# Performance work log

Measured on AMD Instinct MI355X. Metric: run time of the kernel, lower is better.

## Reference

```python
import jax, jax.numpy as jnp
import numpy as np

N_NODES = 100000


def gcn_layer(x, edge_index, W, b):
    """PyG GCNConv: h = D^-1/2 (A+I) D^-1/2 (x W) + b, scatter-sum aggregation."""
    n = x.shape[0]
    h = x @ W  # [N, out]
    loop = jnp.arange(n, dtype=edge_index.dtype)
    src = jnp.concatenate([edge_index[0], loop])  # [E+N]
    dst = jnp.concatenate([edge_index[1], loop])
    deg = jax.ops.segment_sum(jnp.ones_like(dst, dtype=h.dtype), dst, num_segments=n)
    dinv = jnp.where(deg > 0, jax.lax.rsqrt(deg), 0.0)
    norm = dinv[src] * dinv[dst]  # [E+N]
    msg = h[src] * norm[:, None]  # gather + scale (largest intermediate)
    out = jax.ops.segment_sum(msg, dst, num_segments=n)
    return out + b


def setup_inputs() -> dict:
    key = jax.random.key(0)
    k = jax.random.split(key, 8)
    in_dim, hid_dim, out_dim = 128, 64, 112
    E = 1600000
    x = jax.random.normal(k[0], (N_NODES, in_dim), dtype=jnp.float32)
    edge_index = jax.random.randint(k[1], (2, E), 0, N_NODES, dtype=jnp.int32)
    s1 = 1.0 / np.sqrt(in_dim)
    s2 = 1.0 / np.sqrt(hid_dim)
    return {
        "x": x,
        "edge_index": edge_index,
        "W1": jax.random.uniform(k[2], (in_dim, hid_dim), jnp.float32, -s1, s1),
        "b1": jnp.zeros((hid_dim,), jnp.float32),
        "W2": jax.random.uniform(k[3], (hid_dim, hid_dim), jnp.float32, -s2, s2),
        "b2": jnp.zeros((hid_dim,), jnp.float32),
        "W3": jax.random.uniform(k[4], (hid_dim, out_dim), jnp.float32, -s2, s2),
        "b3": jnp.zeros((out_dim,), jnp.float32),
    }


def reference(x, edge_index, W1, b1, W2, b2, W3, b3):
    # eval mode: dropout is identity
    h = jax.nn.relu(gcn_layer(x, edge_index, W1, b1))
    h = jax.nn.relu(gcn_layer(h, edge_index, W2, b2))
    return gcn_layer(h, edge_index, W3, b3)
```

## Files before the change

kernel.cpp:

```cpp
#include <hip/hip_runtime.h>
#include <hip/hip_fp16.h>
#include <math.h>


#define IN_DIM 128
#define HID 64
#define OUT_DIM 112
#define SCAN_TILE 1024
#define LSHIFT 7
#define LMASK 127
#define MAXBUCK 1024
#define CHUNK 8192

__global__ __launch_bounds__(256) void coarse_hist_kernel(const int* __restrict__ dst,
                                                          int* __restrict__ H,
                                                          int E, int nbuck) {
  __shared__ int hist[MAXBUCK];
  for (int i = threadIdx.x; i < nbuck; i += 256) hist[i] = 0;
  __syncthreads();
  int lo = blockIdx.x * CHUNK;
  int hi = min(E, lo + CHUNK);
  for (int i = lo + threadIdx.x; i < hi; i += 256)
    atomicAdd(&hist[dst[i] >> LSHIFT], 1);
  __syncthreads();
  int* Hrow = &H[(size_t)blockIdx.x * nbuck];
  for (int i = threadIdx.x; i < nbuck; i += 256) Hrow[i] = hist[i];
}

__global__ __launch_bounds__(256) void btotal_kernel(const int* __restrict__ H,
                                                     int* __restrict__ btotal,
                                                     int nchunk, int nbuck) {
  int wv = threadIdx.x >> 6, lane = threadIdx.x & 63;
  int b = blockIdx.x * 4 + wv;
  if (b >= nbuck) return;
  int s = 0;
  for (int c = lane; c < nchunk; c += 64) s += H[(size_t)c * nbuck + b];
#pragma unroll
  for (int off = 1; off < 64; off <<= 1) s += __shfl_xor(s, off);
  if (lane == 0) btotal[b] = s;
}

__global__ __launch_bounds__(1024) void bbase_scan_kernel(const int* __restrict__ btotal,
                                                          int* __restrict__ bbase, int nbuck) {
  __shared__ int sh[1024];
  int t = threadIdx.x;
  int v = (t < nbuck) ? btotal[t] : 0;
  sh[t] = v;
  __syncthreads();
  for (int off = 1; off < 1024; off <<= 1) {
    int u = (t >= off) ? sh[t - off] : 0;
    __syncthreads();
    sh[t] += u;
    __syncthreads();
  }
  if (t < nbuck) bbase[t] = sh[t] - v;
  if (t == 1023) bbase[nbuck] = sh[1023];
}

__global__ __launch_bounds__(256) void chunk_offset_kernel(int* __restrict__ H,
                                                           const int* __restrict__ bbase,
                                                           int nchunk, int nbuck) {
  int wv = threadIdx.x >> 6, lane = threadIdx.x & 63;
  int b = blockIdx.x * 4 + wv;
  if (b >= nbuck) return;
  int run = bbase[b];
  for (int c0 = 0; c0 < nchunk; c0 += 64) {
    int c = c0 + lane;
    int v = (c < nchunk) ? H[(size_t)c * nbuck + b] : 0;
    int incl = v;
#pragma unroll
    for (int off = 1; off < 64; off <<= 1) {
      int u = __shfl_up(incl, off);
      if (lane >= off) incl += u;
    }
    if (c < nchunk) H[(size_t)c * nbuck + b] = run + incl - v;
    run += __shfl(incl, 63);
  }
}

__global__ __launch_bounds__(256) void coarse_scatter_kernel(const int* __restrict__ src,
                                                             const int* __restrict__ dst,
                                                             const int* __restrict__ H,
                                                             int* __restrict__ packed,
                                                             int E, int nbuck) {
  __shared__ int cur[MAXBUCK];
  const int* Hrow = &H[(size_t)blockIdx.x * nbuck];
  for (int i = threadIdx.x; i < nbuck; i += 256) cur[i] = Hrow[i];
  __syncthreads();
  int lo = blockIdx.x * CHUNK;
  int hi = min(E, lo + CHUNK);
  for (int i = lo + threadIdx.x; i < hi; i += 256) {
    int s = src[i], d = dst[i];
    int b = d >> LSHIFT;
    int pos = atomicAdd(&cur[b], 1);
    packed[pos] = (s << LSHIFT) | (d & LMASK);
  }
}

__global__ __launch_bounds__(256) void fine_count_kernel(const int* __restrict__ packed,
                                                         const int* __restrict__ bbase,
                                                         int* __restrict__ cnt, int n) {
  int b = blockIdx.x;
  __shared__ int hist[128];
  int t = threadIdx.x;
  if (t < 128) hist[t] = 0;
  __syncthreads();
  int e0 = bbase[b], e1 = bbase[b + 1];
  for (int e = e0 + t; e < e1; e += 256) atomicAdd(&hist[packed[e] & LMASK], 1);
  __syncthreads();
  int node = b * 128 + t;
  if (t < 128 && node < n) cnt[node] = hist[t];
}

__global__ __launch_bounds__(256) void fine_scatter_kernel(const int* __restrict__ packed,
                                                           const int* __restrict__ bbase,
                                                           const int* __restrict__ row_start,
                                                           int* __restrict__ ssrc, int n) {
  int b = blockIdx.x;
  __shared__ int cur[128];
  int t = threadIdx.x;
  if (t < 128) {
    int node = b * 128 + t;
    cur[t] = (node < n) ? row_start[node] : 0;
  }
  __syncthreads();
  int e0 = bbase[b], e1 = bbase[b + 1];
  for (int e = e0 + t; e < e1; e += 256) {
    int p = packed[e];
    int slot = atomicAdd(&cur[p & LMASK], 1);
    ssrc[slot] = p >> LSHIFT;
  }
}

__global__ __launch_bounds__(256) void dinv_kernel(const int* __restrict__ cnt,
                                                   float* __restrict__ dinv, int n) {
  int i = blockIdx.x * 256 + threadIdx.x;
  if (i < n) dinv[i] = 1.0f / sqrtf((float)(cnt[i] + 1));
}


__global__ __launch_bounds__(256) void scan_partial_kernel(const int* __restrict__ cnt,
                                                           int* __restrict__ blocksum,
                                                           int n) {
  int t = threadIdx.x;
  int base = blockIdx.x * SCAN_TILE + t * 4;
  int s = 0;
  if (base + 4 <= n) {
    int4 v = *reinterpret_cast<const int4*>(&cnt[base]);
    s = v.x + v.y + v.z + v.w;
  } else {
    for (int i = 0; i < 4; ++i)
      if (base + i < n) s += cnt[base + i];
  }
#pragma unroll
  for (int off = 1; off < 64; off <<= 1) s += __shfl_xor(s, off);
  __shared__ int wsum[4];
  int lane = t & 63, wv = t >> 6;
  if (lane == 0) wsum[wv] = s;
  __syncthreads();
  if (t == 0) blocksum[blockIdx.x] = wsum[0] + wsum[1] + wsum[2] + wsum[3];
}

__global__ __launch_bounds__(1024) void scan_blocksums_kernel(int* __restrict__ blocksum,
                                                              int* __restrict__ total_out,
                                                              int nb) {
  __shared__ int sh[1024];
  int t = threadIdx.x;
  int v = (t < nb) ? blocksum[t] : 0;
  sh[t] = v;
  __syncthreads();
  for (int off = 1; off < 1024; off <<= 1) {
    int u = (t >= off) ? sh[t - off] : 0;
    __syncthreads();
    sh[t] += u;
    __syncthreads();
  }
  if (t < nb) blocksum[t] = sh[t] - v;
  if (t == 1023) *total_out = sh[1023];
}

__global__ __launch_bounds__(256) void scan_final_kernel(const int* __restrict__ cnt,
                                                         const int* __restrict__ blocksum,
                                                         int* __restrict__ row_start, int n) {
  int t = threadIdx.x;
  int base = blockIdx.x * SCAN_TILE + t * 4;
  int v0 = 0, v1 = 0, v2 = 0, v3 = 0;
  if (base + 4 <= n) {
    int4 v = *reinterpret_cast<const int4*>(&cnt[base]);
    v0 = v.x; v1 = v.y; v2 = v.z; v3 = v.w;
  } else {
    if (base + 0 < n) v0 = cnt[base + 0];
    if (base + 1 < n) v1 = cnt[base + 1];
    if (base + 2 < n) v2 = cnt[base + 2];
    if (base + 3 < n) v3 = cnt[base + 3];
  }
  int s = v0 + v1 + v2 + v3;
  __shared__ int sh[256];
  sh[t] = s;
  __syncthreads();
  for (int off = 1; off < 256; off <<= 1) {
    int u = (t >= off) ? sh[t - off] : 0;
    __syncthreads();
    sh[t] += u;
    __syncthreads();
  }
  int run = blocksum[blockIdx.x] + sh[t] - s;
  int p0 = run, p1 = run + v0, p2 = p1 + v1, p3 = p2 + v2;
  if (base + 4 <= n) {
    *reinterpret_cast<int4*>(&row_start[base]) = make_int4(p0, p1, p2, p3);
  } else {
    if (base + 0 < n) row_start[base + 0] = p0;
    if (base + 1 < n) row_start[base + 1] = p1;
    if (base + 2 < n) row_start[base + 2] = p2;
    if (base + 3 < n) row_start[base + 3] = p3;
  }
}

template <int K, int C, int BK, bool DINV, bool BIAS, bool OUTH>
__global__ __launch_bounds__(256, 4) void gemm_scale_kernel(const float* __restrict__ X,
                                                            const float* __restrict__ W,
                                                            const float* __restrict__ dinv,
                                                            const float* __restrict__ bias,
                                                            void* __restrict__ G, int n) {
  constexpr int Cp = ((C + 63) / 64) * 64;
  constexpr int CQ = Cp / 4;
  constexpr int RG = 256 / CQ;
  constexpr int RPB = RG * 4;
  constexpr int XP = BK + 4;
  constexpr int XQ = BK / 4;
  constexpr int NXQ = RPB * XQ;
  constexpr int NWQ = BK * CQ;

  __shared__ float Xs[RPB * XP];
  __shared__ float Ws[BK * Cp];

  const int tid = threadIdx.x;
  const int rbase = blockIdx.x * RPB;
  const int ct = tid % CQ, rt = tid / CQ;
  const int c0 = ct * 4, r0 = rt * 4;

  float acc[4][4];
#pragma unroll
  for (int a = 0; a < 4; ++a)
#pragma unroll
    for (int b = 0; b < 4; ++b) acc[a][b] = 0.f;

  for (int kb = 0; kb < K; kb += BK) {
    if (kb > 0) __syncthreads();
#pragma unroll
    for (int q = tid; q < NXQ; q += 256) {
      int r = q / XQ, j = q % XQ;
      int grow = rbase + r;
      if (grow >= n) grow = n - 1;
      *reinterpret_cast<float4*>(&Xs[r * XP + j * 4]) =
          *reinterpret_cast<const float4*>(&X[(size_t)grow * K + kb + j * 4]);
    }
#pragma unroll
    for (int q = tid; q < NWQ; q += 256) {
      int k = q / CQ, cq = q % CQ, c = cq * 4;
      float4 v = make_float4(0.f, 0.f, 0.f, 0.f);
      if (c < C) v = *reinterpret_cast<const float4*>(&W[(size_t)(kb + k) * C + c]);
      *reinterpret_cast<float4*>(&Ws[k * Cp + c]) = v;
    }
    __syncthreads();

#pragma unroll 2
    for (int k = 0; k < BK; k += 4) {
      float4 w0 = *reinterpret_cast<const float4*>(&Ws[(k + 0) * Cp + c0]);
      float4 w1 = *reinterpret_cast<const float4*>(&Ws[(k + 1) * Cp + c0]);
      float4 w2 = *reinterpret_cast<const float4*>(&Ws[(k + 2) * Cp + c0]);
      float4 w3 = *reinterpret_cast<const float4*>(&Ws[(k + 3) * Cp + c0]);
#pragma unroll
      for (int rr = 0; rr < 4; ++rr) {
        float4 xv = *reinterpret_cast<const float4*>(&Xs[(r0 + rr) * XP + k]);
        acc[rr][0] = fmaf(xv.w, w3.x, fmaf(xv.z, w2.x, fmaf(xv.y, w1.x, fmaf(xv.x, w0.x, acc[rr][0]))));
        acc[rr][1] = fmaf(xv.w, w3.y, fmaf(xv.z, w2.y, fmaf(xv.y, w1.y, fmaf(xv.x, w0.y, acc[rr][1]))));
        acc[rr][2] = fmaf(xv.w, w3.z, fmaf(xv.z, w2.z, fmaf(xv.y, w1.z, fmaf(xv.x, w0.z, acc[rr][2]))));
        acc[rr][3] = fmaf(xv.w, w3.w, fmaf(xv.z, w2.w, fmaf(xv.y, w1.w, fmaf(xv.x, w0.w, acc[rr][3]))));
      }
    }
  }

#pragma unroll
  for (int rr = 0; rr < 4; ++rr) {
    int row = rbase + r0 + rr;
    if (row < n && c0 < C) {
      float s = DINV ? dinv[row] : 1.0f;
      float4 v;
      v.x = acc[rr][0] * s;
      v.y = acc[rr][1] * s;
      v.z = acc[rr][2] * s;
      v.w = acc[rr][3] * s;
      if (BIAS) {
        float4 bv = *reinterpret_cast<const float4*>(&bias[c0]);
        v.x += bv.x; v.y += bv.y; v.z += bv.z; v.w += bv.w;
      }
      if (OUTH) {
        union { __half2 h2[2]; float2 f2; } u;
        u.h2[0] = __floats2half2_rn(v.x, v.y);
        u.h2[1] = __floats2half2_rn(v.z, v.w);
        *reinterpret_cast<float2*>(&reinterpret_cast<__half*>(G)[(size_t)row * C + c0]) = u.f2;
      } else {
        *reinterpret_cast<float4*>(&reinterpret_cast<float*>(G)[(size_t)row * C + c0]) = v;
      }
    }
  }
}

template <int C, bool RELU, bool BIAS, bool TSCALE, bool OUTH>
__global__ __launch_bounds__(256) void agg_kernel(const __half* __restrict__ g,
                                                  const int* __restrict__ row_start,
                                                  const int* __restrict__ ssrc,
                                                  const float* __restrict__ dinv,
                                                  const float* __restrict__ bias,
                                                  void* __restrict__ out, int n) {
  static_assert(C == 64, "agg assumes 64 channels");
  const int tid = threadIdx.x;
  const int wv = tid >> 6;
  const int lane = tid & 63;
  const int h = lane >> 5;
  const int q = lane & 31;
  int node = blockIdx.x * 4 + wv;
  if (node >= n) return;
  const __half2* g2 = reinterpret_cast<const __half2*>(g);

  int e0 = row_start[node];
  int e1 = row_start[node + 1];
  int deg = e1 - e0;
  float2 acc = make_float2(0.f, 0.f);
  if (h == 0) {
    float2 sv = __half22float2(g2[(size_t)node * 32 + q]);
    acc.x = sv.x; acc.y = sv.y;
  }
  const int pairs = deg >> 1;
  const int base = e0 + h;
  int k = 0;
  for (; k + 8 <= pairs; k += 8) {
    int idx[8];
#pragma unroll
    for (int i = 0; i < 8; ++i) idx[i] = ssrc[base + 2 * (k + i)];
    __half2 v[8];
#pragma unroll
    for (int i = 0; i < 8; ++i) v[i] = g2[(size_t)idx[i] * 32 + q];
#pragma unroll
    for (int i = 0; i < 8; ++i) {
      float2 f = __half22float2(v[i]);
      acc.x += f.x; acc.y += f.y;
    }
  }
  for (; k + 2 <= pairs; k += 2) {
    int i0 = ssrc[base + 2 * k];
    int i1 = ssrc[base + 2 * (k + 1)];
    float2 f0 = __half22float2(g2[(size_t)i0 * 32 + q]);
    float2 f1 = __half22float2(g2[(size_t)i1 * 32 + q]);
    acc.x += f0.x + f1.x; acc.y += f0.y + f1.y;
  }
  for (; k < pairs; ++k) {
    int i0 = ssrc[base + 2 * k];
    float2 f = __half22float2(g2[(size_t)i0 * 32 + q]);
    acc.x += f.x; acc.y += f.y;
  }
  if (deg & 1) {
    if (h == 0) {
      int i0 = ssrc[e1 - 1];
      float2 f = __half22float2(g2[(size_t)i0 * 32 + q]);
      acc.x += f.x; acc.y += f.y;
    }
  }
  acc.x += __shfl_xor(acc.x, 32);
  acc.y += __shfl_xor(acc.y, 32);

  if (h == 0) {
    float di = dinv[node];
    float rx = acc.x * di, ry = acc.y * di;
    if (BIAS) {
      float2 bv = *reinterpret_cast<const float2*>(&bias[2 * q]);
      rx += bv.x; ry += bv.y;
    }
    if (RELU) { rx = fmaxf(rx, 0.f); ry = fmaxf(ry, 0.f); }
    if (TSCALE) { rx *= di; ry *= di; }
    if (OUTH) {
      reinterpret_cast<__half2*>(out)[(size_t)node * 32 + q] = __floats2half2_rn(rx, ry);
    } else {
      reinterpret_cast<float2*>(out)[(size_t)node * 32 + q] = make_float2(rx, ry);
    }
  }
}

extern "C" void kernel_launch(void* const* d_in, const int* in_sizes, int n_in,
                              void* d_out, int out_size, void* d_ws, size_t ws_size,
                              hipStream_t stream) {
  const float* x = (const float*)d_in[0];
  const int* ei = (const int*)d_in[1];
  const float* W1 = (const float*)d_in[2];
  const float* b1 = (const float*)d_in[3];
  const float* W2 = (const float*)d_in[4];
  const float* b2 = (const float*)d_in[5];
  const float* W3 = (const float*)d_in[6];
  const float* b3 = (const float*)d_in[7];
  float* out = (float*)d_out;

  const int n = in_sizes[0] / IN_DIM;
  const int E = in_sizes[1] / 2;
  const int* src = ei;
  const int* dst = ei + E;
  const int nbuck = (n + LMASK) >> LSHIFT;
  const int nchunk = (E + CHUNK - 1) / CHUNK;

  char* p = (char*)d_ws;
  auto alloc = [&](size_t bytes) {
    char* q = p;
    p += (bytes + 255) & ~(size_t)255;
    return q;
  };
  float* dinv = (float*)alloc((size_t)n * 4);
  int* row_start = (int*)alloc((size_t)(n + 1) * 4);
  int* cnt = (int*)alloc((size_t)n * 4);
  int* blocksum = (int*)alloc((size_t)1024 * 4);
  int* btotal = (int*)alloc((size_t)MAXBUCK * 4);
  int* bbase = (int*)alloc((size_t)(MAXBUCK + 1) * 4);
  int* H = (int*)alloc((size_t)nchunk * nbuck * 4);
  int* packed = (int*)alloc((size_t)E * 4);
  int* ssrc = (int*)alloc((size_t)E * 4);
  __half* gh = (__half*)alloc((size_t)n * HID * 2);
  __half* th = (__half*)alloc((size_t)n * HID * 2);
  float* f32b = (float*)alloc((size_t)n * HID * 4);

  const int NB = (n + SCAN_TILE - 1) / SCAN_TILE;
  const int WGRID = (nbuck + 3) / 4;

  coarse_hist_kernel<<<nchunk, 256, 0, stream>>>(dst, H, E, nbuck);
  btotal_kernel<<<WGRID, 256, 0, stream>>>(H, btotal, nchunk, nbuck);
  bbase_scan_kernel<<<1, 1024, 0, stream>>>(btotal, bbase, nbuck);
  chunk_offset_kernel<<<WGRID, 256, 0, stream>>>(H, bbase, nchunk, nbuck);
  coarse_scatter_kernel<<<nchunk, 256, 0, stream>>>(src, dst, H, packed, E, nbuck);
  fine_count_kernel<<<nbuck, 256, 0, stream>>>(packed, bbase, cnt, n);
  dinv_kernel<<<(n + 255) / 256, 256, 0, stream>>>(cnt, dinv, n);
  scan_partial_kernel<<<NB, 256, 0, stream>>>(cnt, blocksum, n);
  scan_blocksums_kernel<<<1, 1024, 0, stream>>>(blocksum, &row_start[n], NB);
  scan_final_kernel<<<NB, 256, 0, stream>>>(cnt, blocksum, row_start, n);
  fine_scatter_kernel<<<nbuck, 256, 0, stream>>>(packed, bbase, row_start, ssrc, n);

  gemm_scale_kernel<IN_DIM, HID, 64, true, false, true><<<(n + 63) / 64, 256, 0, stream>>>(x, W1, dinv, nullptr, gh, n);
  agg_kernel<HID, true, true, false, false><<<(n + 3) / 4, 256, 0, stream>>>(gh, row_start, ssrc, dinv, b1, f32b, n);

  gemm_scale_kernel<HID, HID, 64, true, false, true><<<(n + 63) / 64, 256, 0, stream>>>(f32b, W2, dinv, nullptr, gh, n);
  agg_kernel<HID, true, true, true, true><<<(n + 3) / 4, 256, 0, stream>>>(gh, row_start, ssrc, dinv, b2, th, n);

  agg_kernel<HID, false, false, false, false><<<(n + 3) / 4, 256, 0, stream>>>(th, row_start, ssrc, dinv, nullptr, f32b, n);
  gemm_scale_kernel<HID, OUT_DIM, 32, false, true, false><<<(n + 31) / 32, 256, 0, stream>>>(f32b, W3, dinv, b3, out, n);
}
```

Before: 382.3 us.

## Process four nodes per wavefront in aggregation with shuffled neighbor indices

Each wavefront in the aggregation kernel now handles four destination nodes instead of one. It loads up to 64 neighbor indices per node with a single coalesced read and broadcasts them through lane shuffles. It then issues 16 gathers per node for all four nodes up front, with a fallback path for nodes of degree above 32. The goal is more memory-level parallelism and fewer serial index loads per neighbor, since average degree is about 16. In exchange it uses many more registers, which may lower occupancy, and it does wasted dummy gathers for low-degree nodes.

Result: slower. 395.2 us (+3.4%).

```diff
diff --git a/kernel.cpp b/kernel.cpp
--- a/kernel.cpp
+++ b/kernel.cpp
@@ -313,76 +313,115 @@
                                                   const int* __restrict__ ssrc,
                                                   const float* __restrict__ dinv,
                                                   const float* __restrict__ bias,
-                                                  void* __restrict__ out, int n) {
+                                                  void* __restrict__ out, int n, int E) {
   static_assert(C == 64, "agg assumes 64 channels");
   const int tid = threadIdx.x;
   const int wv = tid >> 6;
   const int lane = tid & 63;
   const int h = lane >> 5;
   const int q = lane & 31;
-  int node = blockIdx.x * 4 + wv;
-  if (node >= n) return;
+  const int wid = blockIdx.x * 4 + wv;
+  const int base = wid * 4;
+  if (base >= n) return;
   const __half2* g2 = reinterpret_cast<const __half2*>(g);
 
-  int e0 = row_start[node];
-  int e1 = row_start[node + 1];
-  int deg = e1 - e0;
-  float2 acc = make_float2(0.f, 0.f);
+  int rs[5];
+#pragma unroll
+  for (int j = 0; j < 5; ++j) rs[j] = row_start[min(base + j, n)];
+  int e0[4], deg[4];
+#pragma unroll
+  for (int j = 0; j < 4; ++j) { e0[j] = rs[j]; deg[j] = rs[j + 1] - rs[j]; }
+
+  int midx[4];
+#pragma unroll
+  for (int j = 0; j < 4; ++j) {
+    int off = (lane < deg[j]) ? lane : (deg[j] > 0 ? deg[j] - 1 : 0);
+    midx[j] = ssrc[min(e0[j] + off, E - 1)];
+  }
+
+  float2 acc[4];
+  float di[4];
+#pragma unroll
+  for (int j = 0; j < 4; ++j) {
+    int node = base + j;
+    int cl = (node < n) ? node : base;
+    float2 sv = __half22float2(g2[(size_t)cl * 32 + q]);
+    acc[j] = (h == 0 && node < n) ? sv : make_float2(0.f, 0.f);
+    di[j] = dinv[cl];
+  }
+
+  __half2 vb[4][16];
+#pragma unroll
+  for (int j = 0; j < 4; ++j) {
+#pragma unroll
+    for (int i = 0; i < 16; ++i) {
+      int t = 2 * i + h;
+      int s = (t < deg[j]) ? __shfl(midx[j], t) : base;
+      vb[j][i] = g2[(size_t)s * 32 + q];
+    }
+  }
+#pragma unroll
+  for (int j = 0; j < 4; ++j) {
+#pragma unroll
+    for (int i = 0; i < 16; ++i) {
+      int t = 2 * i + h;
+      if (t < deg[j]) {
+        float2 f = __half22float2(vb[j][i]);
+        acc[j].x += f.x; acc[j].y += f.y;
+      }
+    }
+  }
+
+#pragma unroll
+  for (int j = 0; j < 4; ++j) {
+    if (deg[j] > 32) {
+      __half2 vc[16];
+#pragma unroll
+      for (int i = 0; i < 16; ++i) {
+        int t = 32 + 2 * i + h;
+        int s = (t < deg[j]) ? __shfl(midx[j], t) : base;
+        vc[i] = g2[(size_t)s * 32 + q];
+      }
+#pragma unroll
+      for (int i = 0; i < 16; ++i) {
+        int t = 32 + 2 * i + h;
+        if (t < deg[j]) {
+          float2 f = __half22float2(vc[i]);
+          acc[j].x += f.x; acc[j].y += f.y;
+        }
+      }
+      for (int t = 64 + h; t < deg[j]; t += 2) {
+        int s = ssrc[e0[j] + t];
+        float2 f = __half22float2(g2[(size_t)s * 32 + q]);
+        acc[j].x += f.x; acc[j].y += f.y;
+      }
+    }
+  }
+
+#pragma unroll
+  for (int j = 0; j < 4; ++j) {
+    acc[j].x += __shfl_xor(acc[j].x, 32);
+    acc[j].y += __shfl_xor(acc[j].y, 32);
+  }
   if (h == 0) {
-    float2 sv = __half22float2(g2[(size_t)node * 32 + q]);
-    acc.x = sv.x; acc.y = sv.y;
-  }
-  const int pairs = deg >> 1;
-  const int base = e0 + h;
-  int k = 0;
-  for (; k + 8 <= pairs; k += 8) {
-    int idx[8];
-#pragma unroll
-    for (int i = 0; i < 8; ++i) idx[i] = ssrc[base + 2 * (k + i)];
-    __half2 v[8];
-#pragma unroll
-    for (int i = 0; i < 8; ++i) v[i] = g2[(size_t)idx[i] * 32 + q];
-#pragma unroll
-    for (int i = 0; i < 8; ++i) {
-      float2 f = __half22float2(v[i]);
-      acc.x += f.x; acc.y += f.y;
-    }
-  }
-  for (; k + 2 <= pairs; k += 2) {
-    int i0 = ssrc[base + 2 * k];
-    int i1 = ssrc[base + 2 * (k + 1)];
-    float2 f0 = __half22float2(g2[(size_t)i0 * 32 + q]);
-    float2 f1 = __half22float2(g2[(size_t)i1 * 32 + q]);
-    acc.x += f0.x + f1.x; acc.y += f0.y + f1.y;
-  }
-  for (; k < pairs; ++k) {
-    int i0 = ssrc[base + 2 * k];
-    float2 f = __half22float2(g2[(size_t)i0 * 32 + q]);
-    acc.x += f.x; acc.y += f.y;
-  }
-  if (deg & 1) {
-    if (h == 0) {
-      int i0 = ssrc[e1 - 1];
-      float2 f = __half22float2(g2[(size_t)i0 * 32 + q]);
-      acc.x += f.x; acc.y += f.y;
-    }
-  }
-  acc.x += __shfl_xor(acc.x, 32);
-  acc.y += __shfl_xor(acc.y, 32);
-
-  if (h == 0) {
-    float di = dinv[node];
-    float rx = acc.x * di, ry = acc.y * di;
-    if (BIAS) {
-      float2 bv = *reinterpret_cast<const float2*>(&bias[2 * q]);
-      rx += bv.x; ry += bv.y;
-    }
-    if (RELU) { rx = fmaxf(rx, 0.f); ry = fmaxf(ry, 0.f); }
-    if (TSCALE) { rx *= di; ry *= di; }
-    if (OUTH) {
-      reinterpret_cast<__half2*>(out)[(size_t)node * 32 + q] = __floats2half2_rn(rx, ry);
-    } else {
-      reinterpret_cast<float2*>(out)[(size_t)node * 32 + q] = make_float2(rx, ry);
+#pragma unroll
+    for (int j = 0; j < 4; ++j) {
+      int node = base + j;
+      if (node < n) {
+        float d = di[j];
+        float rx = acc[j].x * d, ry = acc[j].y * d;
+        if (BIAS) {
+          float2 bv = *reinterpret_cast<const float2*>(&bias[2 * q]);
+          rx += bv.x; ry += bv.y;
+        }
+        if (RELU) { rx = fmaxf(rx, 0.f); ry = fmaxf(ry, 0.f); }
+        if (TSCALE) { rx *= d; ry *= d; }
+        if (OUTH) {
+          reinterpret_cast<__half2*>(out)[(size_t)node * 32 + q] = __floats2half2_rn(rx, ry);
+        } else {
+          reinterpret_cast<float2*>(out)[(size_t)node * 32 + q] = make_float2(rx, ry);
+        }
+      }
     }
   }
 }
@@ -428,6 +467,7 @@
 
   const int NB = (n + SCAN_TILE - 1) / SCAN_TILE;
   const int WGRID = (nbuck + 3) / 4;
+  const int AGRID = (n + 15) / 16;
 
   coarse_hist_kernel<<<nchunk, 256, 0, stream>>>(dst, H, E, nbuck);
   btotal_kernel<<<WGRID, 256, 0, stream>>>(H, btotal, nchunk, nbuck);
@@ -442,11 +482,11 @@
   fine_scatter_kernel<<<nbuck, 256, 0, stream>>>(packed, bbase, row_start, ssrc, n);
 
   gemm_scale_kernel<IN_DIM, HID, 64, true, false, true><<<(n + 63) / 64, 256, 0, stream>>>(x, W1, dinv, nullptr, gh, n);
-  agg_kernel<HID, true, true, false, false><<<(n + 3) / 4, 256, 0, stream>>>(gh, row_start, ssrc, dinv, b1, f32b, n);
+  agg_kernel<HID, true, true, false, false><<<AGRID, 256, 0, stream>>>(gh, row_start, ssrc, dinv, b1, f32b, n, E);
 
   gemm_scale_kernel<HID, HID, 64, true, false, true><<<(n + 63) / 64, 256, 0, stream>>>(f32b, W2, dinv, nullptr, gh, n);
-  agg_kernel<HID, true, true, true, true><<<(n + 3) / 4, 256, 0, stream>>>(gh, row_start, ssrc, dinv, b2, th, n);
-
-  agg_kernel<HID, false, false, false, false><<<(n + 3) / 4, 256, 0, stream>>>(th, row_start, ssrc, dinv, nullptr, f32b, n);
+  agg_kernel<HID, true, true, true, true><<<AGRID, 256, 0, stream>>>(gh, row_start, ssrc, dinv, b2, th, n, E);
+
+  agg_kernel<HID, false, false, false, false><<<AGRID, 256, 0, stream>>>(th, row_start, ssrc, dinv, nullptr, f32b, n, E);
   gemm_scale_kernel<HID, OUT_DIM, 32, false, true, false><<<(n + 31) / 32, 256, 0, stream>>>(f32b, W3, dinv, b3, out, n);
 }
```

## Replace scalar FP32 GEMMs with MFMA fp16 GEMMs and store intermediates in half

Applied to the files above, without the earlier changes.

Swaps the shared-memory FP32 FMA GEMM for a kernel that uses the 16x16x32 fp16 MFMA instruction. Weights are transposed into LDS as fp16, and A fragments are loaded straight from global memory. The aggregation outputs feeding the next GEMM are now written as fp16 rather than fp32, which halves intermediate traffic. This adds fp16 rounding of inputs and weights, which may hurt accuracy. The epilogue writes scalar half or float values instead of vectorised stores.

After: 355.9 us. -6.9%, faster.

```diff
diff --git a/kernel.cpp b/kernel.cpp
--- a/kernel.cpp
+++ b/kernel.cpp
@@ -11,6 +11,9 @@
 #define LMASK 127
 #define MAXBUCK 1024
 #define CHUNK 8192
+
+typedef _Float16 f16x8 __attribute__((ext_vector_type(8)));
+typedef float f32x4 __attribute__((ext_vector_type(4)));
 
 __global__ __launch_bounds__(256) void coarse_hist_kernel(const int* __restrict__ dst,
                                                           int* __restrict__ H,
@@ -216,92 +219,76 @@
   }
 }
 
-template <int K, int C, int BK, bool DINV, bool BIAS, bool OUTH>
-__global__ __launch_bounds__(256, 4) void gemm_scale_kernel(const float* __restrict__ X,
-                                                            const float* __restrict__ W,
-                                                            const float* __restrict__ dinv,
-                                                            const float* __restrict__ bias,
-                                                            void* __restrict__ G, int n) {
-  constexpr int Cp = ((C + 63) / 64) * 64;
-  constexpr int CQ = Cp / 4;
-  constexpr int RG = 256 / CQ;
-  constexpr int RPB = RG * 4;
-  constexpr int XP = BK + 4;
-  constexpr int XQ = BK / 4;
-  constexpr int NXQ = RPB * XQ;
-  constexpr int NWQ = BK * CQ;
-
-  __shared__ float Xs[RPB * XP];
-  __shared__ float Ws[BK * Cp];
+template <int K, int C, bool XH, bool DINV, bool BIAS, bool OUTH>
+__global__ __launch_bounds__(256) void mfma_gemm_kernel(const void* __restrict__ Xv,
+                                                        const float* __restrict__ W,
+                                                        const float* __restrict__ dinv,
+                                                        const float* __restrict__ bias,
+                                                        void* __restrict__ G, int n) {
+  constexpr int KP = K + 8;
+  constexpr int NT = C / 16;
+  constexpr int KS = K / 32;
+  __shared__ _Float16 Wt[C * KP];
 
   const int tid = threadIdx.x;
-  const int rbase = blockIdx.x * RPB;
-  const int ct = tid % CQ, rt = tid / CQ;
-  const int c0 = ct * 4, r0 = rt * 4;
-
-  float acc[4][4];
-#pragma unroll
-  for (int a = 0; a < 4; ++a)
-#pragma unroll
-    for (int b = 0; b < 4; ++b) acc[a][b] = 0.f;
-
-  for (int kb = 0; kb < K; kb += BK) {
-    if (kb > 0) __syncthreads();
-#pragma unroll
-    for (int q = tid; q < NXQ; q += 256) {
-      int r = q / XQ, j = q % XQ;
-      int grow = rbase + r;
-      if (grow >= n) grow = n - 1;
-      *reinterpret_cast<float4*>(&Xs[r * XP + j * 4]) =
-          *reinterpret_cast<const float4*>(&X[(size_t)grow * K + kb + j * 4]);
-    }
-#pragma unroll
-    for (int q = tid; q < NWQ; q += 256) {
-      int k = q / CQ, cq = q % CQ, c = cq * 4;
-      float4 v = make_float4(0.f, 0.f, 0.f, 0.f);
-      if (c < C) v = *reinterpret_cast<const float4*>(&W[(size_t)(kb + k) * C + c]);
-      *reinterpret_cast<float4*>(&Ws[k * Cp + c]) = v;
-    }
-    __syncthreads();
-
-#pragma unroll 2
-    for (int k = 0; k < BK; k += 4) {
-      float4 w0 = *reinterpret_cast<const float4*>(&Ws[(k + 0) * Cp + c0]);
-      float4 w1 = *reinterpret_cast<const float4*>(&Ws[(k + 1) * Cp + c0]);
-      float4 w2 = *reinterpret_cast<const float4*>(&Ws[(k + 2) * Cp + c0]);
-      float4 w3 = *reinterpret_cast<const float4*>(&Ws[(k + 3) * Cp + c0]);
-#pragma unroll
-      for (int rr = 0; rr < 4; ++rr) {
-        float4 xv = *reinterpret_cast<const float4*>(&Xs[(r0 + rr) * XP + k]);
-        acc[rr][0] = fmaf(xv.w, w3.x, fmaf(xv.z, w2.x, fmaf(xv.y, w1.x, fmaf(xv.x, w0.x, acc[rr][0]))));
-        acc[rr][1] = fmaf(xv.w, w3.y, fmaf(xv.z, w2.y, fmaf(xv.y, w1.y, fmaf(xv.x, w0.y, acc[rr][1]))));
-        acc[rr][2] = fmaf(xv.w, w3.z, fmaf(xv.z, w2.z, fmaf(xv.y, w1.z, fmaf(xv.x, w0.z, acc[rr][2]))));
-        acc[rr][3] = fmaf(xv.w, w3.w, fmaf(xv.z, w2.w, fmaf(xv.y, w1.w, fmaf(xv.x, w0.w, acc[rr][3]))));
-      }
-    }
-  }
-
-#pragma unroll
-  for (int rr = 0; rr < 4; ++rr) {
-    int row = rbase + r0 + rr;
-    if (row < n && c0 < C) {
-      float s = DINV ? dinv[row] : 1.0f;
-      float4 v;
-      v.x = acc[rr][0] * s;
-      v.y = acc[rr][1] * s;
-      v.z = acc[rr][2] * s;
-      v.w = acc[rr][3] * s;
-      if (BIAS) {
-        float4 bv = *reinterpret_cast<const float4*>(&bias[c0]);
-        v.x += bv.x; v.y += bv.y; v.z += bv.z; v.w += bv.w;
-      }
-      if (OUTH) {
-        union { __half2 h2[2]; float2 f2; } u;
-        u.h2[0] = __floats2half2_rn(v.x, v.y);
-        u.h2[1] = __floats2half2_rn(v.z, v.w);
-        *reinterpret_cast<float2*>(&reinterpret_cast<__half*>(G)[(size_t)row * C + c0]) = u.f2;
-      } else {
-        *reinterpret_cast<float4*>(&reinterpret_cast<float*>(G)[(size_t)row * C + c0]) = v;
+  for (int idx = tid; idx < K * C; idx += 256) {
+    int k = idx / C, c = idx % C;
+    Wt[c * KP + k] = (_Float16)W[idx];
+  }
+  __syncthreads();
+
+  const int wv = tid >> 6, l = tid & 63;
+  const int rbase = blockIdx.x * 64 + wv * 16;
+  const int kg = (l >> 4) * 8;
+  const int c16 = l & 15;
+
+  int arow = rbase + c16;
+  if (arow >= n) arow = n - 1;
+  f16x8 af[KS];
+  if (XH) {
+    const _Float16* Xh = reinterpret_cast<const _Float16*>(Xv);
+#pragma unroll
+    for (int ks = 0; ks < KS; ++ks)
+      af[ks] = *reinterpret_cast<const f16x8*>(&Xh[(size_t)arow * K + ks * 32 + kg]);
+  } else {
+    const float* Xf = reinterpret_cast<const float*>(Xv);
+#pragma unroll
+    for (int ks = 0; ks < KS; ++ks) {
+      float4 u0 = *reinterpret_cast<const float4*>(&Xf[(size_t)arow * K + ks * 32 + kg]);
+      float4 u1 = *reinterpret_cast<const float4*>(&Xf[(size_t)arow * K + ks * 32 + kg + 4]);
+      f16x8 a;
+      a[0] = (_Float16)u0.x; a[1] = (_Float16)u0.y; a[2] = (_Float16)u0.z; a[3] = (_Float16)u0.w;
+      a[4] = (_Float16)u1.x; a[5] = (_Float16)u1.y; a[6] = (_Float16)u1.z; a[7] = (_Float16)u1.w;
+      af[ks] = a;
+    }
+  }
+
+  f32x4 acc[NT];
+#pragma unroll
+  for (int nt = 0; nt < NT; ++nt) acc[nt] = (f32x4){0.f, 0.f, 0.f, 0.f};
+
+#pragma unroll
+  for (int ks = 0; ks < KS; ++ks) {
+#pragma unroll
+    for (int nt = 0; nt < NT; ++nt) {
+      f16x8 bf = *reinterpret_cast<const f16x8*>(&Wt[(nt * 16 + c16) * KP + ks * 32 + kg]);
+      acc[nt] = __builtin_amdgcn_mfma_f32_16x16x32_f16(af[ks], bf, acc[nt], 0, 0, 0);
+    }
+  }
+
+#pragma unroll
+  for (int r = 0; r < 4; ++r) {
+    int grow = rbase + (l >> 4) * 4 + r;
+    if (grow < n) {
+      float s = DINV ? dinv[grow] : 1.0f;
+#pragma unroll
+      for (int nt = 0; nt < NT; ++nt) {
+        float v = acc[nt][r] * s;
+        if (BIAS) v += bias[nt * 16 + c16];
+        if (OUTH)
+          reinterpret_cast<__half*>(G)[(size_t)grow * C + nt * 16 + c16] = __float2half(v);
+        else
+          reinterpret_cast<float*>(G)[(size_t)grow * C + nt * 16 + c16] = v;
       }
     }
   }
@@ -422,12 +409,14 @@
   int* H = (int*)alloc((size_t)nchunk * nbuck * 4);
   int* packed = (int*)alloc((size_t)E * 4);
   int* ssrc = (int*)alloc((size_t)E * 4);
-  __half* gh = (__half*)alloc((size_t)n * HID * 2);
-  __half* th = (__half*)alloc((size_t)n * HID * 2);
-  float* f32b = (float*)alloc((size_t)n * HID * 4);
+  __half* gh  = (__half*)alloc((size_t)n * HID * 2);
+  __half* h1h = (__half*)alloc((size_t)n * HID * 2);
+  __half* th  = (__half*)alloc((size_t)n * HID * 2);
+  __half* zh  = h1h;
 
   const int NB = (n + SCAN_TILE - 1) / SCAN_TILE;
   const int WGRID = (nbuck + 3) / 4;
+  const int GGRID = (n + 63) / 64;
 
   coarse_hist_kernel<<<nchunk, 256, 0, stream>>>(dst, H, E, nbuck);
   btotal_kernel<<<WGRID, 256, 0, stream>>>(H, btotal, nchunk, nbuck);
@@ -441,12 +430,12 @@
   scan_final_kernel<<<NB, 256, 0, stream>>>(cnt, blocksum, row_start, n);
   fine_scatter_kernel<<<nbuck, 256, 0, stream>>>(packed, bbase, row_start, ssrc, n);
 
-  gemm_scale_kernel<IN_DIM, HID, 64, true, false, true><<<(n + 63) / 64, 256, 0, stream>>>(x, W1, dinv, nullptr, gh, n);
-  agg_kernel<HID, true, true, false, false><<<(n + 3) / 4, 256, 0, stream>>>(gh, row_start, ssrc, dinv, b1, f32b, n);
-
-  gemm_scale_kernel<HID, HID, 64, true, false, true><<<(n + 63) / 64, 256, 0, stream>>>(f32b, W2, dinv, nullptr, gh, n);
+  mfma_gemm_kernel<IN_DIM, HID, false, true, false, true><<<GGRID, 256, 0, stream>>>(x, W1, dinv, nullptr, gh, n);
+  agg_kernel<HID, true, true, false, true><<<(n + 3) / 4, 256, 0, stream>>>(gh, row_start, ssrc, dinv, b1, h1h, n);
+
+  mfma_gemm_kernel<HID, HID, true, true, false, true><<<GGRID, 256, 0, stream>>>(h1h, W2, dinv, nullptr, gh, n);
   agg_kernel<HID, true, true, true, true><<<(n + 3) / 4, 256, 0, stream>>>(gh, row_start, ssrc, dinv, b2, th, n);
 
-  agg_kernel<HID, false, false, false, false><<<(n + 3) / 4, 256, 0, stream>>>(th, row_start, ssrc, dinv, nullptr, f32b, n);
-  gemm_scale_kernel<HID, OUT_DIM, 32, false, true, false><<<(n + 31) / 32, 256, 0, stream>>>(f32b, W3, dinv, b3, out, n);
-}
+  agg_kernel<HID, false, false, false, true><<<(n + 3) / 4, 256, 0, stream>>>(th, row_start, ssrc, dinv, nullptr, zh, n);
+  mfma_gemm_kernel<HID, OUT_DIM, true, false, true, false><<<GGRID, 256, 0, stream>>>(zh, W3, nullptr, b3, out, n);
+}
```
